# Kernel optimization log

Hardware: AMD Instinct MI355X
Metric: run time of the kernel (lower is better)

## Reference

```python
import jax, jax.numpy as jnp
import numpy as np

N = 100000   # nodes
E = 1600000  # edges
D = 128      # input feature dim
H = 128      # hidden dim
L = 3        # gnn layers
G = 64       # graphs in batch
C = 2        # classes


def setup_inputs() -> dict:
    key = jax.random.key(0)
    ks = jax.random.split(key, 12)
    s = 0.05
    x = jax.random.normal(ks[0], (N, D), jnp.float32)
    edge_index = jax.random.randint(ks[1], (2, E), 0, N, dtype=jnp.int32)
    batch = jnp.sort(jax.random.randint(ks[2], (N,), 0, G, dtype=jnp.int32))
    return {
        "x": x,
        "edge_index": edge_index,
        "batch": batch,
        "W0": jax.random.normal(ks[3], (D, H), jnp.float32) * s,
        "b0": jnp.zeros((H,), jnp.float32),
        "Wg": jax.random.normal(ks[4], (L, H, H), jnp.float32) * s,
        "bg": jnp.zeros((L, H), jnp.float32),
        "Wc1": jax.random.normal(ks[5], (H, H), jnp.float32) * s,
        "bc1": jnp.zeros((H,), jnp.float32),
        "Wc2": jax.random.normal(ks[6], (H, C), jnp.float32) * s,
        "bc2": jnp.zeros((C,), jnp.float32),
    }


def reference(x, edge_index, batch, W0, b0, Wg, bg, Wc1, bc1, Wc2, bc2):
    # --- GCN normalization with self-loops (PyG gcn_norm) ---
    src, dst = edge_index[0], edge_index[1]
    loops = jnp.arange(N, dtype=src.dtype)
    src_f = jnp.concatenate([src, loops])  # [E+N] message sources (x_j)
    dst_f = jnp.concatenate([dst, loops])  # [E+N] aggregation targets
    deg = jax.ops.segment_sum(jnp.ones((E + N,), x.dtype), dst_f, num_segments=N)
    dinv = jnp.where(deg > 0, jax.lax.rsqrt(deg), 0.0)
    norm = (dinv[src_f] * dinv[dst_f])[:, None]  # [E+N, 1]

    # --- input linear + relu (dropout is identity in eval mode) ---
    h = jax.nn.relu(x @ W0 + b0)  # [N, H]

    # --- stacked GCNConv layers with residual + relu ---
    for l in range(L):
        xw = h @ Wg[l]  # [N, H]
        agg = jax.ops.segment_sum(xw[src_f] * norm, dst_f, num_segments=N) + bg[l]
        h = jax.nn.relu(h + agg)

    # --- global add pool over graphs ---
    pooled = jax.ops.segment_sum(h, batch, num_segments=G)  # [G, H]

    # --- classifier MLP + softmax ---
    z = jax.nn.relu(pooled @ Wc1 + bc1)
    return jax.nn.softmax(z @ Wc2 + bc2, axis=-1)  # [G, C]
```

## Files before the change

### kernel.cpp

```cpp
#include <hip/hip_runtime.h>

#define NN 100000
#define NE 1600000
#define HD 128
#define NG 64
#define NL 3
#define NBK 391
#define NEB 391
#define CAP 4608
#define NRB 6250
#define FP4_SCALE 8.0f
#define FP4_INV   0.125f

typedef __attribute__((ext_vector_type(8))) short bf16x8;
typedef __attribute__((ext_vector_type(4))) float f32x4;
typedef __attribute__((ext_vector_type(2))) float f32x2;
union U4 { uint4 u; bf16x8 b; };


__device__ __forceinline__ unsigned f2bf(float f) {
    unsigned u = __float_as_uint(f);
    return (u + 0x7FFFu + ((u >> 16) & 1u)) >> 16;
}
__device__ __forceinline__ float bf_lo(unsigned w) { return __uint_as_float(w << 16); }
__device__ __forceinline__ float bf_hi(unsigned w) { return __uint_as_float(w & 0xFFFF0000u); }
__device__ __forceinline__ unsigned cvt_pk_bf16(float lo, float hi) {
    unsigned r;
    asm("v_cvt_pk_bf16_f32 %0, %1, %2" : "=v"(r) : "v"(lo), "v"(hi));
    return r;
}


__global__ __launch_bounds__(256) void k_pre(const float* __restrict__ W0,
                                             const float* __restrict__ Wg,
                                             unsigned* __restrict__ Wb,
                                             const int* __restrict__ src,
                                             const int* __restrict__ dst,
                                             int* __restrict__ gcur,
                                             unsigned* __restrict__ pairs,
                                             const int* __restrict__ batch,
                                             int* __restrict__ start) {
    int blk = blockIdx.x;
    if (blk < 32) {
        int gid = blk * 256 + threadIdx.x;
        for (int i = gid; i < 4 * 8192; i += 32 * 256) {
            int m = i >> 13;
            int r = i & 8191;
            int col = r & 127;
            int p = r >> 7;
            int k0, k1;
            if (m == 0) { k0 = 2 * p; k1 = 2 * p + 1; }
            else        { k0 = p;     k1 = p + 64;    }
            const float* Ws = (m == 0) ? W0 : (Wg + (m - 1) * 16384);
            float w0 = Ws[k0 * 128 + col];
            float w1 = Ws[k1 * 128 + col];
            Wb[m * 8192 + col * 64 + (((2 * p) ^ ((col & 7) << 3)) >> 1)] = (f2bf(w1) << 16) | f2bf(w0);
        }
    } else if (blk < 32 + NEB) {
        __shared__ int cnt[NBK];
        __shared__ int bse[NBK];
        __shared__ int rnk[NBK];
        for (int i = threadIdx.x; i < NBK; i += 256) { cnt[i] = 0; rnk[i] = 0; }
        __syncthreads();
        int base = (blk - 32) * 4096;
        int d[16];
#pragma unroll
        for (int j = 0; j < 16; j++) {
            int e = base + j * 256 + threadIdx.x;
            d[j] = (e < NE) ? dst[e] : -1;
            if (d[j] >= 0) atomicAdd(&cnt[((unsigned)d[j]) >> 8], 1);
        }
        __syncthreads();
        for (int i = threadIdx.x; i < NBK; i += 256) {
            int c = cnt[i];
            bse[i] = c ? atomicAdd(&gcur[i], c) : 0;
        }
        __syncthreads();
#pragma unroll
        for (int j = 0; j < 16; j++) {
            int e = base + j * 256 + threadIdx.x;
            if (e < NE) {
                int b = ((unsigned)d[j]) >> 8;
                int r = atomicAdd(&rnk[b], 1);
                int pos = bse[b] + r;
                if (pos < CAP)
                    pairs[(size_t)b * CAP + pos] = (unsigned)src[e] | (((unsigned)d[j] & 255u) << 17);
            }
        }
    } else {
        int i = (blk - 32 - NEB) * 256 + threadIdx.x;
        if (i >= NN) return;
        int b = batch[i];
        int prev = (i == 0) ? -1 : batch[i - 1];
        for (int g = prev + 1; g <= b; g++) start[g] = i;
        if (i == NN - 1) {
            for (int g = b + 1; g <= NG; g++) start[g] = NN;
        }
    }
}


__global__ __launch_bounds__(256) void k_bfgemm(const unsigned* __restrict__ pairs,
                                                const int* __restrict__ gcur,
                                                int* __restrict__ row_ptr, int* __restrict__ degA,
                                                float* __restrict__ dinv, unsigned* __restrict__ csr,
                                                const float* __restrict__ Xf,
                                                const unsigned* __restrict__ Wb,
                                                const float* __restrict__ bias,
                                                unsigned* __restrict__ hb) {
    __shared__ unsigned short Bt[128 * 128];
    if (blockIdx.x < NBK) {
        int* cnt  = (int*)Bt;
        int* cur  = cnt + 256;
        int* wsum = cur + 256;
        int t = threadIdx.x, k = blockIdx.x;
        int base = k * CAP;
        int ne = min(gcur[k], CAP);
        cnt[t] = 0;
        __syncthreads();
        for (int e = t; e < ne; e += 256) atomicAdd(&cnt[pairs[base + e] >> 17], 1);
        __syncthreads();
        int v = cnt[t];
        int lane = t & 63, wv = t >> 6;
        int sc = v;
#pragma unroll
        for (int off = 1; off < 64; off <<= 1) {
            int n = __shfl_up(sc, off);
            if (lane >= off) sc += n;
        }
        if (lane == 63) wsum[wv] = sc;
        __syncthreads();
        int wbase = 0;
#pragma unroll
        for (int wi = 0; wi < 3; wi++) if (wi < wv) wbase += wsum[wi];
        int excl = base + wbase + sc - v;
        int node = (k << 8) + t;
        if (node < NN) {
            row_ptr[node] = excl;
            degA[node] = v;
            dinv[node] = rsqrtf((float)(v + 1));
        }
        cur[t] = excl;
        __syncthreads();
        for (int e = t; e < ne; e += 256) {
            unsigned p = pairs[base + e];
            int pos = atomicAdd(&cur[p >> 17], 1);
            csr[pos] = (p & 0x1FFFFu) << 6;
        }
        return;
    }

    {
        const uint4* s4 = (const uint4*)Wb;
        uint4* d4 = (uint4*)Bt;
        for (int i = threadIdx.x; i < 2048; i += 256) d4[i] = s4[i];
    }
    __syncthreads();

    int lane = threadIdx.x & 63;
    int l15 = lane & 15, q = lane >> 4;
    int rb = (blockIdx.x - NBK) * 4 + (threadIdx.x >> 6);
    if (rb >= NRB) return;
    int r0 = rb * 16;

    U4 a[4];
    const float* xrow = Xf + (size_t)(r0 + l15) * 128 + q * 8;
#pragma unroll
    for (int kk = 0; kk < 4; kk++) {
        float4 f0 = *(const float4*)(xrow + kk * 32);
        float4 f1 = *(const float4*)(xrow + kk * 32 + 4);
        a[kk].u.x = (f2bf(f0.y) << 16) | f2bf(f0.x);
        a[kk].u.y = (f2bf(f0.w) << 16) | f2bf(f0.z);
        a[kk].u.z = (f2bf(f1.y) << 16) | f2bf(f1.x);
        a[kk].u.w = (f2bf(f1.w) << 16) | f2bf(f1.z);
    }

    f32x4 acc[8];
#pragma unroll
    for (int ct = 0; ct < 8; ct++) acc[ct] = (f32x4){0.f, 0.f, 0.f, 0.f};
#pragma unroll
    for (int kk = 0; kk < 4; kk++) {
#pragma unroll
        for (int ct = 0; ct < 8; ct++) {
            int col = ct * 16 + l15;
            int off = col * 128 + ((kk * 32 + q * 8) ^ ((col & 7) << 3));
            U4 b;
            b.u = *(const uint4*)&Bt[off];
            acc[ct] = __builtin_amdgcn_mfma_f32_16x16x32_bf16(a[kk].b, b.b, acc[ct], 0, 0, 0);
        }
    }

    float bv[8];
#pragma unroll
    for (int ct = 0; ct < 8; ct++) bv[ct] = bias[ct * 16 + l15];
#pragma unroll
    for (int r = 0; r < 4; r++) {
        int row = r0 + q * 4 + r;
#pragma unroll
        for (int ct = 0; ct < 4; ct++) {
            float lo = fmaxf(acc[ct][r] + bv[ct], 0.f);
            float hi = fmaxf(acc[ct + 4][r] + bv[ct + 4], 0.f);
            hb[(size_t)row * 64 + ct * 16 + l15] = cvt_pk_bf16(lo, hi);
        }
    }
}


__global__ __launch_bounds__(256) void k_mgemm1(
    const unsigned* __restrict__ Xb,
    const unsigned* __restrict__ Wb,
    const float* __restrict__ dinv, unsigned* __restrict__ Out) {
    __shared__ unsigned short Bt[128 * 128];
    {
        const uint4* s4 = (const uint4*)Wb;
        uint4* d4 = (uint4*)Bt;
        for (int i = threadIdx.x; i < 2048; i += 256) d4[i] = s4[i];
    }
    __syncthreads();

    int lane = threadIdx.x & 63;
    int l15 = lane & 15, q = lane >> 4;
    int rb = blockIdx.x * 4 + (threadIdx.x >> 6);
    if (rb >= NRB) return;
    int r0 = rb * 16;

    U4 a[4];
    const unsigned* xrow = Xb + (size_t)(r0 + l15) * 64 + q * 4;
#pragma unroll
    for (int kk = 0; kk < 4; kk++) a[kk].u = *(const uint4*)(xrow + kk * 16);

    f32x4 acc[8];
#pragma unroll
    for (int ct = 0; ct < 8; ct++) acc[ct] = (f32x4){0.f, 0.f, 0.f, 0.f};
#pragma unroll
    for (int kk = 0; kk < 4; kk++) {
#pragma unroll
        for (int ct = 0; ct < 8; ct++) {
            int col = ct * 16 + l15;
            int off = col * 128 + ((kk * 32 + q * 8) ^ ((col & 7) << 3));
            U4 b;
            b.u = *(const uint4*)&Bt[off];
            acc[ct] = __builtin_amdgcn_mfma_f32_16x16x32_bf16(a[kk].b, b.b, acc[ct], 0, 0, 0);
        }
    }

#pragma unroll
    for (int r = 0; r < 4; r++) {
        int row = r0 + q * 4 + r;
        float sc = dinv[row] * FP4_SCALE;
        unsigned dw = __builtin_amdgcn_cvt_scalef32_pk_fp4_f32(0u, acc[0][r] * sc, acc[4][r] * sc, 1.0f, 0);
        dw = __builtin_amdgcn_cvt_scalef32_pk_fp4_f32(dw, acc[2][r] * sc, acc[6][r] * sc, 1.0f, 1);
        dw = __builtin_amdgcn_cvt_scalef32_pk_fp4_f32(dw, acc[1][r] * sc, acc[5][r] * sc, 1.0f, 2);
        dw = __builtin_amdgcn_cvt_scalef32_pk_fp4_f32(dw, acc[3][r] * sc, acc[7][r] * sc, 1.0f, 3);
        Out[(size_t)row * 16 + l15] = dw;
    }
}


__global__ __launch_bounds__(256) void k_aggregate(const unsigned char* __restrict__ xb,
                                                   unsigned* __restrict__ hb,
                                                   const int* __restrict__ row_ptr,
                                                   const int* __restrict__ degA,
                                                   const unsigned* __restrict__ csr,
                                                   const float* __restrict__ dinv,
                                                   const float* __restrict__ bg) {
    int wave = threadIdx.x >> 6;
    int lane = threadIdx.x & 63;
    int q = lane >> 4;
    int l16 = lane & 15;
    int sub = l16 >> 3;
    int l8 = l16 & 7;
    int node = blockIdx.x * 16 + wave * 4 + q;
    unsigned e = (unsigned)row_ptr[node];
    unsigned e1 = e + (unsigned)degA[node];
    unsigned loff = (unsigned)l8 * 8u;

    f32x2 p0 = {0.f, 0.f}, p1 = {0.f, 0.f}, p2 = {0.f, 0.f}, p3 = {0.f, 0.f};
    f32x2 q0 = {0.f, 0.f}, q1 = {0.f, 0.f}, q2 = {0.f, 0.f}, q3 = {0.f, 0.f};

#define ACC8(V) \
    p0 += __builtin_amdgcn_cvt_scalef32_pk_f32_fp4((V).x, 1.0f, 0); \
    p1 += __builtin_amdgcn_cvt_scalef32_pk_f32_fp4((V).x, 1.0f, 1); \
    p2 += __builtin_amdgcn_cvt_scalef32_pk_f32_fp4((V).x, 1.0f, 2); \
    p3 += __builtin_amdgcn_cvt_scalef32_pk_f32_fp4((V).x, 1.0f, 3); \
    q0 += __builtin_amdgcn_cvt_scalef32_pk_f32_fp4((V).y, 1.0f, 0); \
    q1 += __builtin_amdgcn_cvt_scalef32_pk_f32_fp4((V).y, 1.0f, 1); \
    q2 += __builtin_amdgcn_cvt_scalef32_pk_f32_fp4((V).y, 1.0f, 2); \
    q3 += __builtin_amdgcn_cvt_scalef32_pk_f32_fp4((V).y, 1.0f, 3);

    for (; e + 7 < e1; e += 8) {
        unsigned o0 = csr[e + sub];
        unsigned o1 = csr[e + 2 + sub];
        unsigned o2 = csr[e + 4 + sub];
        unsigned o3 = csr[e + 6 + sub];
        uint2 v0 = *(const uint2*)(xb + (o0 + loff));
        uint2 v1 = *(const uint2*)(xb + (o1 + loff));
        uint2 v2 = *(const uint2*)(xb + (o2 + loff));
        uint2 v3 = *(const uint2*)(xb + (o3 + loff));
        ACC8(v0); ACC8(v1); ACC8(v2); ACC8(v3);
    }
    if (e + 3 < e1) {
        unsigned o0 = csr[e + sub];
        unsigned o1 = csr[e + 2 + sub];
        uint2 v0 = *(const uint2*)(xb + (o0 + loff));
        uint2 v1 = *(const uint2*)(xb + (o1 + loff));
        ACC8(v0); ACC8(v1);
        e += 4;
    }
    if (e + 1 < e1) {
        unsigned o = csr[e + sub];
        uint2 v = *(const uint2*)(xb + (o + loff));
        ACC8(v);
        e += 2;
    }
    if (e + (unsigned)sub < e1) {
        unsigned o = csr[e + sub];
        uint2 v = *(const uint2*)(xb + (o + loff));
        ACC8(v);
    }
#undef ACC8

    f32x2 s0 = sub ? q0 : p0;
    f32x2 s1 = sub ? q1 : p1;
    f32x2 s2 = sub ? q2 : p2;
    f32x2 s3 = sub ? q3 : p3;
    f32x2 t0 = sub ? p0 : q0;
    f32x2 t1 = sub ? p1 : q1;
    f32x2 t2 = sub ? p2 : q2;
    f32x2 t3 = sub ? p3 : q3;
    s0.x += __shfl_xor(t0.x, 8); s0.y += __shfl_xor(t0.y, 8);
    s1.x += __shfl_xor(t1.x, 8); s1.y += __shfl_xor(t1.y, 8);
    s2.x += __shfl_xor(t2.x, 8); s2.y += __shfl_xor(t2.y, 8);
    s3.x += __shfl_xor(t3.x, 8); s3.y += __shfl_xor(t3.y, 8);

    int j_e = 2 * l8 + sub;

    unsigned ovd = *(const unsigned*)(xb + (((unsigned)node << 6) + (unsigned)j_e * 4u));
    s0 += __builtin_amdgcn_cvt_scalef32_pk_f32_fp4(ovd, 1.0f, 0);
    s1 += __builtin_amdgcn_cvt_scalef32_pk_f32_fp4(ovd, 1.0f, 1);
    s2 += __builtin_amdgcn_cvt_scalef32_pk_f32_fp4(ovd, 1.0f, 2);
    s3 += __builtin_amdgcn_cvt_scalef32_pk_f32_fp4(ovd, 1.0f, 3);

    float di2 = dinv[node] * FP4_INV;
    float a[8] = {s0.x, s0.y, s1.x, s1.y, s2.x, s2.y, s3.x, s3.y};
    size_t hbase = (size_t)node * 64;
    unsigned hv0 = hb[hbase + j_e];
    unsigned hv1 = hb[hbase + j_e + 32];
    unsigned hv2 = hb[hbase + j_e + 16];
    unsigned hv3 = hb[hbase + j_e + 48];
    float hh[8] = {bf_lo(hv0), bf_hi(hv0), bf_lo(hv1), bf_hi(hv1),
                   bf_lo(hv2), bf_hi(hv2), bf_lo(hv3), bf_hi(hv3)};
    float gg[8] = {bg[j_e], bg[j_e + 64], bg[j_e + 32], bg[j_e + 96],
                   bg[j_e + 16], bg[j_e + 80], bg[j_e + 48], bg[j_e + 112]};
    float r[8];
#pragma unroll
    for (int i = 0; i < 8; i++) r[i] = fmaxf(hh[i] + di2 * a[i] + gg[i], 0.f);
    hb[hbase + j_e]      = cvt_pk_bf16(r[0], r[1]);
    hb[hbase + j_e + 32] = cvt_pk_bf16(r[2], r[3]);
    hb[hbase + j_e + 16] = cvt_pk_bf16(r[4], r[5]);
    hb[hbase + j_e + 48] = cvt_pk_bf16(r[6], r[7]);
}


__global__ __launch_bounds__(128) void k_pool(const unsigned* __restrict__ hb,
                                              const int* __restrict__ start,
                                              float* __restrict__ pooled) {
    int g = blockIdx.x >> 4;
    int c = blockIdx.x & 15;
    int s = start[g], e = start[g + 1];
    int len = e - s;
    if (len <= 0) return;
    int chunk = (len + 15) >> 4;
    int r0 = s + c * chunk;
    int r1 = min(e, r0 + chunk);
    if (r0 >= r1) return;
    int jj = threadIdx.x & 63;
    int half = threadIdx.x >> 6;
    float ax = 0.f, ay = 0.f;
    for (int r = r0 + half; r < r1; r += 2) {
        unsigned v = hb[(size_t)r * 64 + jj];
        ax += bf_lo(v);
        ay += bf_hi(v);
    }
    atomicAdd(&pooled[g * 128 + jj], ax);
    atomicAdd(&pooled[g * 128 + jj + 64], ay);
}


__global__ __launch_bounds__(128) void k_classify(const float* __restrict__ pooled,
                                                  const float* __restrict__ Wc1,
                                                  const float* __restrict__ bc1,
                                                  const float* __restrict__ Wc2,
                                                  const float* __restrict__ bc2,
                                                  float* __restrict__ out) {
    __shared__ float p[128];
    __shared__ float r0s[128];
    __shared__ float r1s[128];
    int g = blockIdx.x;
    int j = threadIdx.x;
    p[j] = pooled[g * 128 + j];
    __syncthreads();
    float acc = bc1[j];
#pragma unroll 4
    for (int k = 0; k < 128; k++) acc = fmaf(p[k], Wc1[k * 128 + j], acc);
    float z = fmaxf(acc, 0.f);
    r0s[j] = z * Wc2[j * 2 + 0];
    r1s[j] = z * Wc2[j * 2 + 1];
    __syncthreads();
    for (int st = 64; st > 0; st >>= 1) {
        if (j < st) { r0s[j] += r0s[j + st]; r1s[j] += r1s[j + st]; }
        __syncthreads();
    }
    if (j == 0) {
        float l0 = r0s[0] + bc2[0];
        float l1 = r1s[0] + bc2[1];
        float m = fmaxf(l0, l1);
        float e0 = expf(l0 - m), e1 = expf(l1 - m);
        float inv = 1.f / (e0 + e1);
        out[g * 2 + 0] = e0 * inv;
        out[g * 2 + 1] = e1 * inv;
    }
}


extern "C" void kernel_launch(void* const* d_in, const int* in_sizes, int n_in,
                              void* d_out, int out_size, void* d_ws, size_t ws_size,
                              hipStream_t stream) {
    (void)in_sizes; (void)n_in; (void)out_size;

    const float* x     = (const float*)d_in[0];
    const int*   ei    = (const int*)d_in[1];
    const int*   batch = (const int*)d_in[2];
    const float* W0    = (const float*)d_in[3];
    const float* b0    = (const float*)d_in[4];
    const float* Wg    = (const float*)d_in[5];
    const float* bg    = (const float*)d_in[6];
    const float* Wc1   = (const float*)d_in[7];
    const float* bc1   = (const float*)d_in[8];
    const float* Wc2   = (const float*)d_in[9];
    const float* bc2   = (const float*)d_in[10];
    float* out = (float*)d_out;

    const int* srcp = ei;
    const int* dstp = ei + NE;

    char* w = (char*)d_ws;
    auto alloc = [&](size_t bytes) {
        char* p = w;
        w += (bytes + 255) & ~(size_t)255;
        return p;
    };
    int*      gcur    = (int*)alloc((size_t)NBK * 4);
    float*    pooled  = (float*)alloc((size_t)NG * HD * 4);
    size_t zbytes = (size_t)((char*)w - (char*)gcur);
    unsigned* hb      = (unsigned*)alloc((size_t)NN * 64 * 4);
    unsigned* xws4    = (unsigned*)alloc((size_t)NN * 16 * 4);
    float*    dinv    = (float*)alloc((size_t)NN * 4);
    int*      row_ptr = (int*)alloc((size_t)NN * 4);
    int*      degA    = (int*)alloc((size_t)NN * 4);
    unsigned* csr     = (unsigned*)alloc((size_t)NBK * CAP * 4);
    unsigned* pairs   = (unsigned*)alloc((size_t)NBK * CAP * 4);
    unsigned* Wb      = (unsigned*)alloc((size_t)4 * 8192 * 4);
    int*      start   = (int*)alloc((NG + 1) * 4);
    if ((size_t)(w - (char*)d_ws) > ws_size) return;

    hipMemsetAsync(gcur, 0, zbytes, stream);

    k_pre<<<32 + NEB + 391, 256, 0, stream>>>(W0, Wg, Wb, srcp, dstp, gcur, pairs, batch, start);

    int gb = (NRB + 3) / 4;
    k_bfgemm<<<NBK + gb, 256, 0, stream>>>(pairs, gcur, row_ptr, degA, dinv, csr,
                                           x, Wb, b0, hb);
    for (int l = 0; l < NL; l++) {
        k_mgemm1<<<gb, 256, 0, stream>>>(hb, Wb + (size_t)(l + 1) * 8192, dinv, xws4);
        k_aggregate<<<NRB, 256, 0, stream>>>((const unsigned char*)xws4, hb, row_ptr, degA, csr, dinv, bg + l * HD);
    }
    k_pool<<<NG * 16, 128, 0, stream>>>(hb, start, pooled);
    k_classify<<<NG, 128, 0, stream>>>(pooled, Wc1, bc1, Wc2, bc2, out);
}
```

Before: 213.3 us.

## Fuse next-layer GEMM into aggregate kernel epilogue with double-buffered FP4 output

Each aggregate block (16 nodes) now stages its new bf16 hidden rows in LDS and has wave 0 run the next layer's 16x128x128 MFMA GEMM, writing FP4-scaled messages into a second buffer. This removes two separate k_mgemm1 launches and the re-read of h from global memory. The two message buffers alternate so the gather for the current layer never reads rows being overwritten. The cost is a block-wide barrier, extra LDS, and a serial GEMM tail on one wave while the other three waves idle.

```diff
diff --git a/kernel.cpp b/kernel.cpp
--- a/kernel.cpp
+++ b/kernel.cpp
@@ -257,13 +257,17 @@
 }
 
 
+template <int FUSE>
 __global__ __launch_bounds__(256) void k_aggregate(const unsigned char* __restrict__ xb,
                                                    unsigned* __restrict__ hb,
                                                    const int* __restrict__ row_ptr,
                                                    const int* __restrict__ degA,
                                                    const unsigned* __restrict__ csr,
                                                    const float* __restrict__ dinv,
-                                                   const float* __restrict__ bg) {
+                                                   const float* __restrict__ bg,
+                                                   const unsigned short* __restrict__ WbN,
+                                                   unsigned* __restrict__ OutNext) {
+    __shared__ unsigned tile[16][64];
     int wave = threadIdx.x >> 6;
     int lane = threadIdx.x & 63;
     int q = lane >> 4;
@@ -355,10 +359,59 @@
     float r[8];
 #pragma unroll
     for (int i = 0; i < 8; i++) r[i] = fmaxf(hh[i] + di2 * a[i] + gg[i], 0.f);
-    hb[hbase + j_e]      = cvt_pk_bf16(r[0], r[1]);
-    hb[hbase + j_e + 32] = cvt_pk_bf16(r[2], r[3]);
-    hb[hbase + j_e + 16] = cvt_pk_bf16(r[4], r[5]);
-    hb[hbase + j_e + 48] = cvt_pk_bf16(r[6], r[7]);
+    unsigned w0 = cvt_pk_bf16(r[0], r[1]);
+    unsigned w1 = cvt_pk_bf16(r[2], r[3]);
+    unsigned w2 = cvt_pk_bf16(r[4], r[5]);
+    unsigned w3 = cvt_pk_bf16(r[6], r[7]);
+    hb[hbase + j_e]      = w0;
+    hb[hbase + j_e + 32] = w1;
+    hb[hbase + j_e + 16] = w2;
+    hb[hbase + j_e + 48] = w3;
+
+    if (FUSE) {
+        int nl = wave * 4 + q;
+        unsigned sw = (unsigned)(nl << 2) & 63u;
+        tile[nl][(unsigned)j_e ^ sw]        = w0;
+        tile[nl][(unsigned)(j_e + 32) ^ sw] = w1;
+        tile[nl][(unsigned)(j_e + 16) ^ sw] = w2;
+        tile[nl][(unsigned)(j_e + 48) ^ sw] = w3;
+        __syncthreads();
+        if (wave != 0) return;
+
+        int l15 = lane & 15;
+        int qq = lane >> 4;
+        unsigned swr = (unsigned)(l15 << 2) & 63u;
+        U4 a2[4];
+#pragma unroll
+        for (int kk = 0; kk < 4; kk++) {
+            unsigned d = (unsigned)(kk * 16 + qq * 4) ^ swr;
+            a2[kk].u = *(const uint4*)&tile[l15][d];
+        }
+        f32x4 acc2[8];
+#pragma unroll
+        for (int ct = 0; ct < 8; ct++) acc2[ct] = (f32x4){0.f, 0.f, 0.f, 0.f};
+#pragma unroll
+        for (int kk = 0; kk < 4; kk++) {
+#pragma unroll
+            for (int ct = 0; ct < 8; ct++) {
+                int col = ct * 16 + l15;
+                int off = col * 128 + ((kk * 32 + qq * 8) ^ ((col & 7) << 3));
+                U4 b;
+                b.u = *(const uint4*)&WbN[off];
+                acc2[ct] = __builtin_amdgcn_mfma_f32_16x16x32_bf16(a2[kk].b, b.b, acc2[ct], 0, 0, 0);
+            }
+        }
+#pragma unroll
+        for (int rr = 0; rr < 4; rr++) {
+            int row = blockIdx.x * 16 + qq * 4 + rr;
+            float sc = dinv[row] * FP4_SCALE;
+            unsigned dw = __builtin_amdgcn_cvt_scalef32_pk_fp4_f32(0u, acc2[0][rr] * sc, acc2[4][rr] * sc, 1.0f, 0);
+            dw = __builtin_amdgcn_cvt_scalef32_pk_fp4_f32(dw, acc2[2][rr] * sc, acc2[6][rr] * sc, 1.0f, 1);
+            dw = __builtin_amdgcn_cvt_scalef32_pk_fp4_f32(dw, acc2[1][rr] * sc, acc2[5][rr] * sc, 1.0f, 2);
+            dw = __builtin_amdgcn_cvt_scalef32_pk_fp4_f32(dw, acc2[3][rr] * sc, acc2[7][rr] * sc, 1.0f, 3);
+            OutNext[(size_t)row * 16 + l15] = dw;
+        }
+    }
 }
 
 
@@ -454,7 +507,8 @@
     float*    pooled  = (float*)alloc((size_t)NG * HD * 4);
     size_t zbytes = (size_t)((char*)w - (char*)gcur);
     unsigned* hb      = (unsigned*)alloc((size_t)NN * 64 * 4);
-    unsigned* xws4    = (unsigned*)alloc((size_t)NN * 16 * 4);
+    unsigned* xwsA    = (unsigned*)alloc((size_t)NN * 16 * 4);
+    unsigned* xwsB    = (unsigned*)alloc((size_t)NN * 16 * 4);
     float*    dinv    = (float*)alloc((size_t)NN * 4);
     int*      row_ptr = (int*)alloc((size_t)NN * 4);
     int*      degA    = (int*)alloc((size_t)NN * 4);
@@ -471,10 +525,15 @@
     int gb = (NRB + 3) / 4;
     k_bfgemm<<<NBK + gb, 256, 0, stream>>>(pairs, gcur, row_ptr, degA, dinv, csr,
                                            x, Wb, b0, hb);
-    for (int l = 0; l < NL; l++) {
-        k_mgemm1<<<gb, 256, 0, stream>>>(hb, Wb + (size_t)(l + 1) * 8192, dinv, xws4);
-        k_aggregate<<<NRB, 256, 0, stream>>>((const unsigned char*)xws4, hb, row_ptr, degA, csr, dinv, bg + l * HD);
-    }
+    k_mgemm1<<<gb, 256, 0, stream>>>(hb, Wb + (size_t)1 * 8192, dinv, xwsA);
+    k_aggregate<1><<<NRB, 256, 0, stream>>>((const unsigned char*)xwsA, hb, row_ptr, degA, csr,
+                                            dinv, bg + 0 * HD,
+                                            (const unsigned short*)(Wb + (size_t)2 * 8192), xwsB);
+    k_aggregate<1><<<NRB, 256, 0, stream>>>((const unsigned char*)xwsB, hb, row_ptr, degA, csr,
+                                            dinv, bg + 1 * HD,
+                                            (const unsigned short*)(Wb + (size_t)3 * 8192), xwsA);
+    k_aggregate<0><<<NRB, 256, 0, stream>>>((const unsigned char*)xwsA, hb, row_ptr, degA, csr,
+                                            dinv, bg + 2 * HD, nullptr, nullptr);
     k_pool<<<NG * 16, 128, 0, stream>>>(hb, start, pooled);
     k_classify<<<NG, 128, 0, stream>>>(pooled, Wc1, bc1, Wc2, bc2, out);
 }
```

New measurement: 228.1 us. 7.0% more time.
